# Optimization experiments

Hardware: AMD Instinct MI355X
Metric: run time of the kernel (lower is better)

Reference implementation:

```python
import jax, jax.numpy as jnp
import numpy as np

N = 8192
F_IN = 128
D = 128
NEG_SLOPE = 0.2  # cfg.negativeslope (standard GAT value)
MASK_FILL = -9e15


def setup_inputs() -> dict:
    key = jax.random.key(0)
    k1, k2, k3, k4 = jax.random.split(key, 4)
    A = jax.random.randint(k1, (N, N), 0, 2, dtype=jnp.int32)
    X = jax.random.normal(k2, (N, F_IN), dtype=jnp.float32)
    # glorot init for Ws, xavier_uniform(gain=1.414) for a
    lim_w = float(np.sqrt(6.0 / (F_IN + D)))
    Ws = jax.random.uniform(k3, (F_IN, D), minval=-lim_w, maxval=lim_w, dtype=jnp.float32)
    lim_a = 1.414 * float(np.sqrt(6.0 / (2 * D + 1)))
    a = jax.random.uniform(k4, (2 * D, 1), minval=-lim_a, maxval=lim_a, dtype=jnp.float32)
    return {"A": A, "X": X, "Ws": Ws, "a": a}


def reference(A, X, Ws, a):
    # Wh: [N, D]
    Wh = X @ Ws
    d = Wh.shape[-1]
    # additive attention: e_ij = leaky_relu(Wh_i . a1 + Wh_j . a2)
    e1 = Wh @ a[:d]          # [N, 1]
    e2 = Wh @ a[d:]          # [N, 1]
    e = jax.nn.leaky_relu(e1 + e2.T, negative_slope=NEG_SLOPE)  # [N, N]
    e = jnp.where(A > 0, e, MASK_FILL)
    attn = jax.nn.softmax(e, axis=1)  # row-wise over neighbors
    H = attn @ Wh            # [N, D]
    return H
```

## Files before the change

### kernel.cpp

```cpp
#include <hip/hip_runtime.h>
#include <hip/hip_bf16.h>

#define NN 8192
#define DD 128

typedef __attribute__((ext_vector_type(8))) short short8;
typedef __attribute__((ext_vector_type(4))) float f32x4;
typedef unsigned int u32;

__device__ __forceinline__ ushort f2bf(float f) {
    __hip_bfloat16 h = __float2bfloat16(f);
    return *(ushort*)&h;
}

__device__ __forceinline__ void async_ld16(const void* g, void* l) {
    __builtin_amdgcn_global_load_lds(
        (const __attribute__((address_space(1))) u32*)g,
        (__attribute__((address_space(3))) u32*)l, 16, 0, 0);
}

__global__ __launch_bounds__(256) void k1_gemm(const float* __restrict__ X,
                                               const float* __restrict__ Ws,
                                               float* __restrict__ Wh) {
    __shared__ float lWs[128 * 132];
    __shared__ float lX[32 * 132];
    int t = threadIdx.x, bx = blockIdx.x;
    const float4* Ws4 = (const float4*)Ws;
    const float4* X4 = (const float4*)X;
    for (int j = 0; j < 16; ++j) {
        int u = j * 256 + t;
        int k = u >> 5, c4 = u & 31;
        *(float4*)&lWs[k * 132 + c4 * 4] = Ws4[u];
    }
    for (int j = 0; j < 4; ++j) {
        int u = j * 256 + t;
        int r = u >> 5, c4 = u & 31;
        *(float4*)&lX[r * 132 + c4 * 4] = X4[bx * 1024 + u];
    }
    __syncthreads();
    int r0 = (t >> 5) * 4, c0 = (t & 31) * 4;
    float acc[4][4];
#pragma unroll
    for (int i = 0; i < 4; ++i)
#pragma unroll
        for (int j = 0; j < 4; ++j) acc[i][j] = 0.f;
#pragma unroll 4
    for (int k = 0; k < 128; ++k) {
        float4 wv = *(const float4*)&lWs[k * 132 + c0];
        float x0 = lX[(r0 + 0) * 132 + k];
        float x1 = lX[(r0 + 1) * 132 + k];
        float x2 = lX[(r0 + 2) * 132 + k];
        float x3 = lX[(r0 + 3) * 132 + k];
#pragma unroll
        for (int j = 0; j < 4; ++j) {
            acc[0][j] += x0 * ((const float*)&wv)[j];
            acc[1][j] += x1 * ((const float*)&wv)[j];
            acc[2][j] += x2 * ((const float*)&wv)[j];
            acc[3][j] += x3 * ((const float*)&wv)[j];
        }
    }
#pragma unroll
    for (int i = 0; i < 4; ++i)
        *(float4*)&Wh[(size_t)(bx * 32 + r0 + i) * 128 + c0] =
            (float4){acc[i][0], acc[i][1], acc[i][2], acc[i][3]};
}

__global__ __launch_bounds__(256) void k2_prep(const float* __restrict__ Wh,
                                               const float* __restrict__ a,
                                               ushort* __restrict__ WhT,
                                               float* __restrict__ C1,
                                               float* __restrict__ C1s,
                                               float* __restrict__ E2p,
                                               float* __restrict__ E2n) {
    __shared__ float lT[128 * 65];
    __shared__ float la[256];
    int t = threadIdx.x;
    int i0 = blockIdx.x * 64;
    la[t] = a[t];
    for (int j = 0; j < 32; ++j) {
        int u = j * 256 + t;
        int r = u >> 7, c = u & 127;
        lT[c * 65 + r] = Wh[(size_t)(i0 + r) * 128 + c];
    }
    __syncthreads();
    int r = t >> 2, q = t & 3;
    float s1 = 0.f, s2 = 0.f;
    for (int j = 0; j < 32; ++j) {
        int d = q * 32 + j;
        float v = lT[d * 65 + r];
        s1 += v * la[d];
        s2 += v * la[128 + d];
    }
    s1 += __shfl_xor(s1, 1); s1 += __shfl_xor(s1, 2);
    s2 += __shfl_xor(s2, 1); s2 += __shfl_xor(s2, 2);
    if (q == 0) {
        int i = i0 + r;
        C1[i]  = __expf(s1);
        C1s[i] = __expf(0.2f * s1);
        E2p[i] = __expf(s2);
        E2n[i] = __expf(0.2f * s2);
    }
    int d = t >> 1, hf = t & 1;
    __attribute__((aligned(16))) ushort tmp[32];
#pragma unroll
    for (int s = 0; s < 32; ++s) tmp[s] = f2bf(lT[d * 65 + hf * 32 + s]);
    uint4* dst = (uint4*)&WhT[(size_t)d * NN + i0 + hf * 32];
    const uint4* srcv = (const uint4*)tmp;
#pragma unroll
    for (int s = 0; s < 4; ++s) dst[s] = srcv[s];
}

__global__ __launch_bounds__(1024, 4) void k3_main(
    const int* __restrict__ A, const ushort* __restrict__ WhT,
    const float* __restrict__ C1, const float* __restrict__ C1s,
    const float* __restrict__ E2p, const float* __restrict__ E2n,
    float* __restrict__ Hp, float* __restrict__ Lp) {

    __shared__ __align__(16) char lB[2 * 32768];
    __shared__ __align__(16) char lA[2 * 32768];

    int tid = threadIdx.x;
    int lane = tid & 63;
    int wv = tid >> 6;
    int g = wv & 3;
    int h = wv >> 2;
    int n = lane & 15;
    int kg = lane >> 4;

    int bx = blockIdx.x;
    int kb = blockIdx.y;
    int row = bx * 64 + g * 16 + n;

    float c1 = C1[row], c1s = C1s[row];

    int p0 = wv * 2;
    int tp0 = p0 >> 3, cp0 = p0 & 7;
    int tp1 = (p0 + 1) >> 3, cp1 = (p0 + 1) & 7;
    int ga0 = p0 >> 3, ta0 = (p0 >> 1) & 3, qa0 = p0 & 1;
    int ga1 = (p0 + 1) >> 3, ta1 = ((p0 + 1) >> 1) & 3, qa1 = (p0 + 1) & 1;

    const ushort* srcB0 = WhT + (size_t)(cp0 * 16 + n) * NN + tp0 * 32 + kg * 8;
    const ushort* srcB1 = WhT + (size_t)(cp1 * 16 + n) * NN + tp1 * 32 + kg * 8;
    const int* srcA0 = A + (size_t)(bx * 64 + ga0 * 16 + n) * NN + ta0 * 32 + kg * 8 + qa0 * 4;
    const int* srcA1 = A + (size_t)(bx * 64 + ga1 * 16 + n) * NN + ta1 * 32 + kg * 8 + qa1 * 4;
    char* dstB0 = lB + p0 * 1024 + lane * 16;
    char* dstB1 = lB + (p0 + 1) * 1024 + lane * 16;
    char* dstA0 = lA + p0 * 1024 + lane * 16;
    char* dstA1 = lA + (p0 + 1) * 1024 + lane * 16;

    const size_t kbase = (size_t)kb * 2048;

    short8 ones;
#pragma unroll
    for (int j = 0; j < 8; ++j) ones[j] = (short)0x3F80;

    f32x4 acc0 = (f32x4){0.f, 0.f, 0.f, 0.f};
    f32x4 acc1 = (f32x4){0.f, 0.f, 0.f, 0.f};
    f32x4 accl = (f32x4){0.f, 0.f, 0.f, 0.f};

    {
        size_t k0 = kbase;
        async_ld16(srcB0 + k0, dstB0);
        async_ld16(srcB1 + k0, dstB1);
        async_ld16(srcA0 + k0, dstA0);
        async_ld16(srcA1 + k0, dstA1);
    }
    __syncthreads();

    for (int kt = 0; kt < 16; ++kt) {
        int b = kt & 1;
        if (kt < 15) {
            size_t kn = kbase + (kt + 1) * 128;
            int bo = (b ^ 1) * 32768;
            async_ld16(srcB0 + kn, dstB0 + bo);
            async_ld16(srcB1 + kn, dstB1 + bo);
            async_ld16(srcA0 + kn, dstA0 + bo);
            async_ld16(srcA1 + kn, dstA1 + bo);
        }
        const char* bufA = lA + b * 32768;
        const char* bufB = lB + b * 32768;
#pragma unroll
        for (int tp = 0; tp < 4; ++tp) {
            const int4* areg = (const int4*)(bufA + (g * 8 + tp * 2) * 1024);
            int4 a0 = areg[lane];
            int4 a1 = areg[64 + lane];
            int kgl = (int)kbase + kt * 128 + tp * 32 + kg * 8;
            float4 pa = *(const float4*)(E2p + kgl);
            float4 pb = *(const float4*)(E2p + kgl + 4);
            float4 na = *(const float4*)(E2n + kgl);
            float4 nb = *(const float4*)(E2n + kgl + 4);
            int am[8]; float ep[8], en[8];
            *(int4*)(am) = a0;     *(int4*)(am + 4) = a1;
            *(float4*)(ep) = pa;   *(float4*)(ep + 4) = pb;
            *(float4*)(en) = na;   *(float4*)(en + 4) = nb;
            short8 af;
#pragma unroll
            for (int u = 0; u < 8; ++u) {
                float w = fmaxf(c1 * ep[u], c1s * en[u]);
                w = am[u] ? w : 0.f;
                af[u] = (short)f2bf(w);
            }
            const short8* bb = (const short8*)(bufB + tp * 8192);
            acc0 = __builtin_amdgcn_mfma_f32_16x16x32_bf16(af, bb[(2 * h + 0) * 64 + lane], acc0, 0, 0, 0);
            acc1 = __builtin_amdgcn_mfma_f32_16x16x32_bf16(af, bb[(2 * h + 1) * 64 + lane], acc1, 0, 0, 0);
            accl = __builtin_amdgcn_mfma_f32_16x16x32_bf16(af, ones, accl, 0, 0, 0);
        }
        __syncthreads();
    }

    if (h == 0 && n == 0) {
#pragma unroll
        for (int r = 0; r < 4; ++r)
            Lp[(size_t)kb * NN + bx * 64 + g * 16 + kg * 4 + r] = accl[r];
    }
    float* Hpb = Hp + (size_t)kb * (NN * DD);
#pragma unroll
    for (int r = 0; r < 4; ++r) {
        int orow = bx * 64 + g * 16 + kg * 4 + r;
        Hpb[(size_t)orow * DD + h * 32 + n] = acc0[r];
        Hpb[(size_t)orow * DD + h * 32 + 16 + n] = acc1[r];
    }
}

__global__ void k4_final(const float* __restrict__ Hp, const float* __restrict__ Lp,
                         float* __restrict__ out) {
    int idx = blockIdx.x * 256 + threadIdx.x;
    int i = idx >> 7;
    float sv = Hp[idx] + Hp[1048576 + idx] + Hp[2097152 + idx] + Hp[3145728 + idx];
    float l = Lp[i] + Lp[8192 + i] + Lp[16384 + i] + Lp[24576 + i];
    out[idx] = sv / l;
}

extern "C" void kernel_launch(void* const* d_in, const int* in_sizes, int n_in,
                              void* d_out, int out_size, void* d_ws, size_t ws_size,
                              hipStream_t stream) {
    const int*   A  = (const int*)d_in[0];
    const float* X  = (const float*)d_in[1];
    const float* Ws = (const float*)d_in[2];
    const float* a  = (const float*)d_in[3];
    float* out = (float*)d_out;

    char* ws = (char*)d_ws;
    float*  Wh  = (float*)(ws);
    ushort* WhT = (ushort*)(ws + (4u << 20));
    float*  C1  = (float*)(ws + (6u << 20));
    float*  C1s = (float*)(ws + (6u << 20) + (32u << 10));
    float*  E2p = (float*)(ws + (6u << 20) + (96u << 10));
    float*  E2n = (float*)(ws + (6u << 20) + (128u << 10));
    float*  Hp  = (float*)(ws + (8u << 20));
    float*  Lp  = (float*)(ws + (24u << 20));

    k1_gemm<<<256, 256, 0, stream>>>(X, Ws, Wh);
    k2_prep<<<128, 256, 0, stream>>>(Wh, a, WhT, C1, C1s, E2p, E2n);
    k3_main<<<dim3(128, 4), 1024, 0, stream>>>(A, WhT, C1, C1s, E2p, E2n, Hp, Lp);
    k4_final<<<4096, 256, 0, stream>>>(Hp, Lp, out);
}
```

Baseline: 462.3 us.

## Fuse GEMM with prep, load adjacency directly to registers, pack E2 as bf16 in LDS

The projection GEMM and the prep kernel are merged, so Wh is transposed in LDS and written straight out as bf16 WhT plus the exp coefficients, with no fp32 Wh round trip and one fewer launch. In the main kernel the adjacency tile is read from global memory directly into registers rather than staged through LDS. The E2 exponentials are packed as bf16 pairs and cached once per block in LDS. The k-step shrinks to 64 so LDS use drops, and launch bounds now ask for 8 blocks per SM. The risks are less latency hiding on the direct A loads and bf16 rounding of E2.

```diff
diff --git a/kernel.cpp b/kernel.cpp
--- a/kernel.cpp
+++ b/kernel.cpp
@@ -11,6 +11,9 @@
 __device__ __forceinline__ ushort f2bf(float f) {
     __hip_bfloat16 h = __float2bfloat16(f);
     return *(ushort*)&h;
+}
+__device__ __forceinline__ float asf(u32 u) {
+    union { u32 i; float f; } v; v.i = u; return v.f;
 }
 
 __device__ __forceinline__ void async_ld16(const void* g, void* l) {
@@ -19,14 +22,18 @@
         (__attribute__((address_space(3))) u32*)l, 16, 0, 0);
 }
 
-__global__ __launch_bounds__(256) void k1_gemm(const float* __restrict__ X,
-                                               const float* __restrict__ Ws,
-                                               float* __restrict__ Wh) {
+__global__ __launch_bounds__(256) void k1_fused(
+    const float* __restrict__ X, const float* __restrict__ Ws,
+    const float* __restrict__ a, ushort* __restrict__ WhT,
+    float* __restrict__ C1, float* __restrict__ C1s, u32* __restrict__ E2bf) {
     __shared__ float lWs[128 * 132];
     __shared__ float lX[32 * 132];
+    __shared__ float la[256];
     int t = threadIdx.x, bx = blockIdx.x;
+    int i0 = bx * 32;
     const float4* Ws4 = (const float4*)Ws;
     const float4* X4 = (const float4*)X;
+    la[t] = a[t];
     for (int j = 0; j < 16; ++j) {
         int u = j * 256 + t;
         int k = u >> 5, c4 = u & 31;
@@ -59,65 +66,51 @@
             acc[3][j] += x3 * ((const float*)&wv)[j];
         }
     }
+    __syncthreads();
+    float* lT = lWs;
 #pragma unroll
     for (int i = 0; i < 4; ++i)
-        *(float4*)&Wh[(size_t)(bx * 32 + r0 + i) * 128 + c0] =
-            (float4){acc[i][0], acc[i][1], acc[i][2], acc[i][3]};
-}
-
-__global__ __launch_bounds__(256) void k2_prep(const float* __restrict__ Wh,
-                                               const float* __restrict__ a,
-                                               ushort* __restrict__ WhT,
-                                               float* __restrict__ C1,
-                                               float* __restrict__ C1s,
-                                               float* __restrict__ E2p,
-                                               float* __restrict__ E2n) {
-    __shared__ float lT[128 * 65];
-    __shared__ float la[256];
-    int t = threadIdx.x;
-    int i0 = blockIdx.x * 64;
-    la[t] = a[t];
-    for (int j = 0; j < 32; ++j) {
-        int u = j * 256 + t;
-        int r = u >> 7, c = u & 127;
-        lT[c * 65 + r] = Wh[(size_t)(i0 + r) * 128 + c];
-    }
-    __syncthreads();
-    int r = t >> 2, q = t & 3;
-    float s1 = 0.f, s2 = 0.f;
-    for (int j = 0; j < 32; ++j) {
-        int d = q * 32 + j;
-        float v = lT[d * 65 + r];
-        s1 += v * la[d];
-        s2 += v * la[128 + d];
-    }
-    s1 += __shfl_xor(s1, 1); s1 += __shfl_xor(s1, 2);
-    s2 += __shfl_xor(s2, 1); s2 += __shfl_xor(s2, 2);
-    if (q == 0) {
-        int i = i0 + r;
-        C1[i]  = __expf(s1);
-        C1s[i] = __expf(0.2f * s1);
-        E2p[i] = __expf(s2);
-        E2n[i] = __expf(0.2f * s2);
+#pragma unroll
+        for (int j = 0; j < 4; ++j) lT[(c0 + j) * 33 + r0 + i] = acc[i][j];
+    __syncthreads();
+    if (t < 128) {
+        int r = t >> 2, q = t & 3;
+        float s1 = 0.f, s2 = 0.f;
+        for (int j = 0; j < 32; ++j) {
+            int d = q * 32 + j;
+            float v = lT[d * 33 + r];
+            s1 += v * la[d];
+            s2 += v * la[128 + d];
+        }
+        s1 += __shfl_xor(s1, 1); s1 += __shfl_xor(s1, 2);
+        s2 += __shfl_xor(s2, 1); s2 += __shfl_xor(s2, 2);
+        if (q == 0) {
+            int i = i0 + r;
+            C1[i]  = __expf(s1);
+            C1s[i] = __expf(0.2f * s1);
+            u32 pe = (u32)f2bf(__expf(s2));
+            u32 ne = (u32)f2bf(__expf(0.2f * s2));
+            E2bf[i] = pe | (ne << 16);
+        }
     }
     int d = t >> 1, hf = t & 1;
-    __attribute__((aligned(16))) ushort tmp[32];
-#pragma unroll
-    for (int s = 0; s < 32; ++s) tmp[s] = f2bf(lT[d * 65 + hf * 32 + s]);
-    uint4* dst = (uint4*)&WhT[(size_t)d * NN + i0 + hf * 32];
+    __attribute__((aligned(16))) ushort tmp[16];
+#pragma unroll
+    for (int s = 0; s < 16; ++s) tmp[s] = f2bf(lT[d * 33 + hf * 16 + s]);
+    uint4* dst = (uint4*)&WhT[(size_t)d * NN + i0 + hf * 16];
     const uint4* srcv = (const uint4*)tmp;
-#pragma unroll
-    for (int s = 0; s < 4; ++s) dst[s] = srcv[s];
-}
-
-__global__ __launch_bounds__(1024, 4) void k3_main(
+    dst[0] = srcv[0];
+    dst[1] = srcv[1];
+}
+
+__global__ __launch_bounds__(1024, 8) void k3_main(
     const int* __restrict__ A, const ushort* __restrict__ WhT,
     const float* __restrict__ C1, const float* __restrict__ C1s,
-    const float* __restrict__ E2p, const float* __restrict__ E2n,
-    float* __restrict__ Hp, float* __restrict__ Lp) {
-
-    __shared__ __align__(16) char lB[2 * 32768];
-    __shared__ __align__(16) char lA[2 * 32768];
+    const u32* __restrict__ E2bf, float* __restrict__ Hp,
+    float* __restrict__ Lp) {
+
+    __shared__ __align__(16) ushort lB[2][16][64][8];
+    __shared__ u32 lE[2048];
 
     int tid = threadIdx.x;
     int lane = tid & 63;
@@ -130,25 +123,18 @@
     int bx = blockIdx.x;
     int kb = blockIdx.y;
     int row = bx * 64 + g * 16 + n;
+    int kbase = kb * 2048;
+
+    lE[tid] = E2bf[kbase + tid];
+    lE[tid + 1024] = E2bf[kbase + tid + 1024];
 
     float c1 = C1[row], c1s = C1s[row];
-
-    int p0 = wv * 2;
-    int tp0 = p0 >> 3, cp0 = p0 & 7;
-    int tp1 = (p0 + 1) >> 3, cp1 = (p0 + 1) & 7;
-    int ga0 = p0 >> 3, ta0 = (p0 >> 1) & 3, qa0 = p0 & 1;
-    int ga1 = (p0 + 1) >> 3, ta1 = ((p0 + 1) >> 1) & 3, qa1 = (p0 + 1) & 1;
-
-    const ushort* srcB0 = WhT + (size_t)(cp0 * 16 + n) * NN + tp0 * 32 + kg * 8;
-    const ushort* srcB1 = WhT + (size_t)(cp1 * 16 + n) * NN + tp1 * 32 + kg * 8;
-    const int* srcA0 = A + (size_t)(bx * 64 + ga0 * 16 + n) * NN + ta0 * 32 + kg * 8 + qa0 * 4;
-    const int* srcA1 = A + (size_t)(bx * 64 + ga1 * 16 + n) * NN + ta1 * 32 + kg * 8 + qa1 * 4;
-    char* dstB0 = lB + p0 * 1024 + lane * 16;
-    char* dstB1 = lB + (p0 + 1) * 1024 + lane * 16;
-    char* dstA0 = lA + p0 * 1024 + lane * 16;
-    char* dstA1 = lA + (p0 + 1) * 1024 + lane * 16;
-
-    const size_t kbase = (size_t)kb * 2048;
+    const int* Arow = A + (size_t)row * NN + kbase + kg * 8;
+
+    int cc_s = wv & 7, tp_s = wv >> 3;
+    const ushort* srcB = WhT + (size_t)(cc_s * 16 + n) * NN + kbase + tp_s * 32 + kg * 8;
+    ushort* dstB0 = &lB[0][cc_s * 2 + tp_s][lane][0];
+    ushort* dstB1 = &lB[1][cc_s * 2 + tp_s][lane][0];
 
     short8 ones;
 #pragma unroll
@@ -158,51 +144,41 @@
     f32x4 acc1 = (f32x4){0.f, 0.f, 0.f, 0.f};
     f32x4 accl = (f32x4){0.f, 0.f, 0.f, 0.f};
 
-    {
-        size_t k0 = kbase;
-        async_ld16(srcB0 + k0, dstB0);
-        async_ld16(srcB1 + k0, dstB1);
-        async_ld16(srcA0 + k0, dstA0);
-        async_ld16(srcA1 + k0, dstA1);
-    }
-    __syncthreads();
-
-    for (int kt = 0; kt < 16; ++kt) {
+    async_ld16(srcB, dstB0);
+    __syncthreads();
+
+    for (int kt = 0; kt < 32; ++kt) {
         int b = kt & 1;
-        if (kt < 15) {
-            size_t kn = kbase + (kt + 1) * 128;
-            int bo = (b ^ 1) * 32768;
-            async_ld16(srcB0 + kn, dstB0 + bo);
-            async_ld16(srcB1 + kn, dstB1 + bo);
-            async_ld16(srcA0 + kn, dstA0 + bo);
-            async_ld16(srcA1 + kn, dstA1 + bo);
-        }
-        const char* bufA = lA + b * 32768;
-        const char* bufB = lB + b * 32768;
-#pragma unroll
-        for (int tp = 0; tp < 4; ++tp) {
-            const int4* areg = (const int4*)(bufA + (g * 8 + tp * 2) * 1024);
-            int4 a0 = areg[lane];
-            int4 a1 = areg[64 + lane];
-            int kgl = (int)kbase + kt * 128 + tp * 32 + kg * 8;
-            float4 pa = *(const float4*)(E2p + kgl);
-            float4 pb = *(const float4*)(E2p + kgl + 4);
-            float4 na = *(const float4*)(E2n + kgl);
-            float4 nb = *(const float4*)(E2n + kgl + 4);
-            int am[8]; float ep[8], en[8];
-            *(int4*)(am) = a0;     *(int4*)(am + 4) = a1;
-            *(float4*)(ep) = pa;   *(float4*)(ep + 4) = pb;
-            *(float4*)(en) = na;   *(float4*)(en + 4) = nb;
+        const int* Ak = Arow + kt * 64;
+        int4 a00 = *(const int4*)(Ak);
+        int4 a01 = *(const int4*)(Ak + 4);
+        int4 a10 = *(const int4*)(Ak + 32);
+        int4 a11 = *(const int4*)(Ak + 36);
+        if (kt < 31)
+            async_ld16(srcB + (kt + 1) * 64, b ? dstB0 : dstB1);
+#pragma unroll
+        for (int tp = 0; tp < 2; ++tp) {
+            int ke = kt * 64 + tp * 32 + kg * 8;
+            uint4 e0 = *(const uint4*)&lE[ke];
+            uint4 e1 = *(const uint4*)&lE[ke + 4];
+            int am[8];
+            *(int4*)(am) = tp ? a10 : a00;
+            *(int4*)(am + 4) = tp ? a11 : a01;
+            u32 ev[8];
+            *(uint4*)(ev) = e0; *(uint4*)(ev + 4) = e1;
             short8 af;
 #pragma unroll
             for (int u = 0; u < 8; ++u) {
-                float w = fmaxf(c1 * ep[u], c1s * en[u]);
+                float ep = asf(ev[u] << 16);
+                float en = asf(ev[u] & 0xFFFF0000u);
+                float w = fmaxf(c1 * ep, c1s * en);
                 w = am[u] ? w : 0.f;
                 af[u] = (short)f2bf(w);
             }
-            const short8* bb = (const short8*)(bufB + tp * 8192);
-            acc0 = __builtin_amdgcn_mfma_f32_16x16x32_bf16(af, bb[(2 * h + 0) * 64 + lane], acc0, 0, 0, 0);
-            acc1 = __builtin_amdgcn_mfma_f32_16x16x32_bf16(af, bb[(2 * h + 1) * 64 + lane], acc1, 0, 0, 0);
+            short8 b0 = *(const short8*)&lB[b][(2 * h + 0) * 2 + tp][lane][0];
+            short8 b1 = *(const short8*)&lB[b][(2 * h + 1) * 2 + tp][lane][0];
+            acc0 = __builtin_amdgcn_mfma_f32_16x16x32_bf16(af, b0, acc0, 0, 0, 0);
+            acc1 = __builtin_amdgcn_mfma_f32_16x16x32_bf16(af, b1, acc1, 0, 0, 0);
             accl = __builtin_amdgcn_mfma_f32_16x16x32_bf16(af, ones, accl, 0, 0, 0);
         }
         __syncthreads();
@@ -241,17 +217,14 @@
     float* out = (float*)d_out;
 
     char* ws = (char*)d_ws;
-    float*  Wh  = (float*)(ws);
-    ushort* WhT = (ushort*)(ws + (4u << 20));
-    float*  C1  = (float*)(ws + (6u << 20));
-    float*  C1s = (float*)(ws + (6u << 20) + (32u << 10));
-    float*  E2p = (float*)(ws + (6u << 20) + (96u << 10));
-    float*  E2n = (float*)(ws + (6u << 20) + (128u << 10));
-    float*  Hp  = (float*)(ws + (8u << 20));
-    float*  Lp  = (float*)(ws + (24u << 20));
-
-    k1_gemm<<<256, 256, 0, stream>>>(X, Ws, Wh);
-    k2_prep<<<128, 256, 0, stream>>>(Wh, a, WhT, C1, C1s, E2p, E2n);
-    k3_main<<<dim3(128, 4), 1024, 0, stream>>>(A, WhT, C1, C1s, E2p, E2n, Hp, Lp);
+    ushort* WhT  = (ushort*)(ws);
+    float*  C1   = (float*)(ws + (2u << 20));
+    float*  C1s  = (float*)(ws + (2u << 20) + (32u << 10));
+    u32*    E2bf = (u32*)(ws + (2u << 20) + (64u << 10));
+    float*  Lp   = (float*)(ws + (2u << 20) + (96u << 10));
+    float*  Hp   = (float*)(ws + (4u << 20));
+
+    k1_fused<<<256, 256, 0, stream>>>(X, Ws, a, WhT, C1, C1s, E2bf);
+    k3_main<<<dim3(128, 4), 1024, 0, stream>>>(A, WhT, C1, C1s, E2bf, Hp, Lp);
     k4_final<<<4096, 256, 0, stream>>>(Hp, Lp, out);
 }
```

Result: no change. 463.8 us (+0.3%).
